# Optimization experiments

Measured on AMD Instinct MI355X. Metric: run time of the kernel, lower is better.

The kernel has to match this reference:

```python
import jax, jax.numpy as jnp
import numpy as np

LATENT = 256
OUT_CH = 1
K = 16
HEADS = 64


def _conv1x1(x, W, b):
    # x: [B, Cin, ...spatial], W: [Cout, Cin], b: [Cout]
    y = jnp.einsum('oc,bc...->bo...', W, x)
    return y + b.reshape((1, -1) + (1,) * (y.ndim - 2))


def _batch_gather(x, idx):
    # x: [B, C, N], idx: [B, Nq, K] -> [B, C, Nq, K]
    return jax.vmap(lambda xb, ib: xb[:, ib])(x, idx)


def setup_inputs() -> dict:
    key = jax.random.key(0)
    ks = jax.random.split(key, 16)
    B, N, NQ = 2, 10000, 10000
    inp = {
        'latents': jax.random.normal(ks[0], (B, LATENT, N), jnp.float32),
        'pts': jax.random.normal(ks[1], (B, 3, N), jnp.float32),
        'pts_query': jax.random.normal(ks[2], (B, 3, NQ), jnp.float32),
        'proj_ids': jax.random.randint(ks[3], (B, NQ, K), 0, N, jnp.int64),
    }
    def lin(k, o, i):
        s = 1.0 / np.sqrt(i)
        k1, k2 = jax.random.split(k)
        return (jax.random.uniform(k1, (o, i), jnp.float32, -s, s),
                jax.random.uniform(k2, (o,), jnp.float32, -s, s))
    inp['W1'], inp['b1'] = lin(ks[4], LATENT, LATENT + 3)
    inp['W2'], inp['b2'] = lin(ks[5], LATENT, LATENT)
    inp['W3'], inp['b3'] = lin(ks[6], LATENT, LATENT)
    inp['Wq'], inp['bq'] = lin(ks[7], HEADS, LATENT)
    inp['Wv'], inp['bv'] = lin(ks[8], LATENT, LATENT)
    inp['W8'], inp['b8'] = lin(ks[9], OUT_CH, LATENT)
    return inp


def reference(latents, pts, pts_query, proj_ids,
              W1, b1, W2, b2, W3, b3, Wq, bq, Wv, bv, W8, b8):
    # gather neighbor latents and points: [B, C, Nq, K], [B, 3, Nq, K]
    x = _batch_gather(latents, proj_ids)
    npts = _batch_gather(pts, proj_ids)
    rel = pts_query[:, :, :, None] - npts          # [B, 3, Nq, K]
    x = jnp.concatenate([x, rel], axis=1)          # [B, C+3, Nq, K]
    x = jax.nn.relu(_conv1x1(x, W1, b1))
    x = jax.nn.relu(_conv1x1(x, W2, b2))
    x = jax.nn.relu(_conv1x1(x, W3, b3))
    query = _conv1x1(x, Wq, bq)                    # [B, 64, Nq, K]
    value = _conv1x1(x, Wv, bv)                    # [B, C, Nq, K]
    attention = jax.nn.softmax(query, axis=-1).mean(axis=1)  # [B, Nq, K]
    # weighted sum over K neighbors: [B, Nq, C] -> [B, C, Nq]
    x = jnp.einsum('bnk,bcnk->bcn', attention, value)
    x = _conv1x1(x, W8, b8)                        # [B, out_ch, Nq]
    return x
```

## Files before the change

### kernel.cpp

```cpp
#include <hip/hip_runtime.h>
#include <cstdint>
#include <cstddef>


#define NLAT 256
#define KNB 16
#define QB 4
#define MROWS 64
#define ROWB 528
#define MTSTR 16896

typedef float    f32x4  __attribute__((ext_vector_type(4)));
typedef float    f32x16 __attribute__((ext_vector_type(16)));
typedef _Float16 f16x8  __attribute__((ext_vector_type(8)));
typedef _Float16 f16x4  __attribute__((ext_vector_type(4)));

struct Smem {
  unsigned char buf[MROWS * ROWB];
  float Sp[4][MROWS];
  float Sv[MROWS];
  int sidx[MROWS];
  int is64;
};

__device__ __forceinline__ void layer_mfma32(
    unsigned char* __restrict__ buf, const unsigned short* __restrict__ Wp,
    const float* __restrict__ bias, int lane, int wave, bool relu)
{
  const int lm32 = lane & 31, h = lane >> 5;
  const char* bp = (const char*)buf + lm32 * 528 + h * 16;
  const char* wbase = (const char*)Wp + (wave * 64 + lm32) * 32 + h * 16;

  f32x16 acc[2][2];
#pragma unroll
  for (int i = 0; i < 2; ++i)
#pragma unroll
    for (int j = 0; j < 2; ++j) acc[i][j] = (f32x16)(0.f);

#pragma unroll
  for (int ks = 0; ks < 16; ++ks) {
    f16x8 a[2], b[2];
#pragma unroll
    for (int ct = 0; ct < 2; ++ct)
      a[ct] = *(const f16x8*)(wbase + ks * 8192 + ct * 1024);
#pragma unroll
    for (int mt = 0; mt < 2; ++mt)
      b[mt] = *(const f16x8*)(bp + mt * MTSTR + ks * 32);
#pragma unroll
    for (int ct = 0; ct < 2; ++ct)
#pragma unroll
      for (int mt = 0; mt < 2; ++mt)
        acc[ct][mt] = __builtin_amdgcn_mfma_f32_32x32x16_f16(a[ct], b[mt], acc[ct][mt], 0, 0, 0);
  }
  __syncthreads();
#pragma unroll
  for (int ct = 0; ct < 2; ++ct) {
#pragma unroll
    for (int q = 0; q < 4; ++q) {
      const int ch0 = wave * 64 + ct * 32 + q * 8 + h * 4;
      const float4 bs = *(const float4*)(bias + ch0);
      const float bb[4] = {bs.x, bs.y, bs.z, bs.w};
#pragma unroll
      for (int mt = 0; mt < 2; ++mt) {
        f16x4 v;
#pragma unroll
        for (int j = 0; j < 4; ++j) {
          float x = acc[ct][mt][q * 4 + j] + bb[j];
          if (relu) x = fmaxf(x, 0.f);
          v[j] = (_Float16)x;
        }
        *(f16x4*)((char*)buf + (mt * 32 + lm32) * 528 + ch0 * 2) = v;
      }
    }
  }
}

extern "C" __global__ __launch_bounds__(256, 4)
void interp_mfma(const float* __restrict__ pts,
                 const float* __restrict__ ptsq,
                 const void*  __restrict__ proj,
                 const unsigned short* __restrict__ L1pre,
                 const float* __restrict__ w1rT,
                 const unsigned short* __restrict__ W2p,
                 const unsigned short* __restrict__ W3p,
                 const unsigned short* __restrict__ Wqh,
                 const float* __restrict__ b2, const float* __restrict__ b3,
                 const float* __restrict__ bq,
                 const float* __restrict__ wv8, const float* __restrict__ c0p,
                 float* __restrict__ out,
                 int N, int NQ)
{
  __shared__ Smem sm;
  const int tid = threadIdx.x;
  const int bid = blockIdx.x;
  const int lane = tid & 63, wave = tid >> 6;
  const int lm = lane & 15, lk = lane >> 4;

  if (tid == 0) {
    const int* p = (const int*)proj;
    int z = 1;
    for (int i = 0; i < 64; ++i) z &= (p[2 * i + 1] == 0);
    sm.is64 = z;
  }
  __syncthreads();
  if (tid < MROWS) {
    long long g = (long long)bid * QB + (tid >> 4);
    long long base = g * KNB + (tid & 15);
    sm.sidx[tid] = sm.is64 ? (int)((const long long*)proj)[base]
                           : ((const int*)proj)[base];
  }
  __syncthreads();

  {
    const int row = tid & 63, part = tid >> 6;
    const int id = sm.sidx[row];
    const long long g = (long long)bid * QB + (row >> 4);
    const int b = (int)(g / NQ);
    const int nq = (int)(g - (long long)b * NQ);
    float rel[3];
#pragma unroll
    for (int j = 0; j < 3; ++j)
      rel[j] = ptsq[((size_t)b * 3 + j) * NQ + nq]
             - pts[((size_t)b * 3 + j) * N + id];
    const _Float16* lp = (const _Float16*)L1pre + ((size_t)b * N + id) * NLAT + part * 64;
    const float* wr0 = w1rT + part * 64;
    const float* wr1 = w1rT + 256 + part * 64;
    const float* wr2 = w1rT + 512 + part * 64;
    char* dst = (char*)sm.buf + row * 528 + part * 128;
#pragma unroll
    for (int cc = 0; cc < 8; ++cc) {
      f16x8 v = *(const f16x8*)(lp + cc * 8);
      const float4 a0 = *(const float4*)(wr0 + cc * 8), a1 = *(const float4*)(wr0 + cc * 8 + 4);
      const float4 b0 = *(const float4*)(wr1 + cc * 8), b1_ = *(const float4*)(wr1 + cc * 8 + 4);
      const float4 c0 = *(const float4*)(wr2 + cc * 8), c1 = *(const float4*)(wr2 + cc * 8 + 4);
      const float wa[8] = {a0.x, a0.y, a0.z, a0.w, a1.x, a1.y, a1.z, a1.w};
      const float wb[8] = {b0.x, b0.y, b0.z, b0.w, b1_.x, b1_.y, b1_.z, b1_.w};
      const float wc[8] = {c0.x, c0.y, c0.z, c0.w, c1.x, c1.y, c1.z, c1.w};
      f16x8 o;
#pragma unroll
      for (int e = 0; e < 8; ++e) {
        float x = (float)v[e] + rel[0] * wa[e] + rel[1] * wb[e] + rel[2] * wc[e];
        o[e] = (_Float16)fmaxf(x, 0.f);
      }
      *(f16x8*)(dst + cc * 16) = o;
    }
  }
  __syncthreads();

  layer_mfma32(sm.buf, W2p, b2, lane, wave, true);
  __syncthreads();
  layer_mfma32(sm.buf, W3p, b3, lane, wave, true);
  __syncthreads();

  const char* bp16 = (const char*)sm.buf + lm * 528 + lk * 16;
  f32x4 qacc[4];
#pragma unroll
  for (int mt = 0; mt < 4; ++mt) qacc[mt] = (f32x4){0.f, 0.f, 0.f, 0.f};
  {
    const char* wqb = (const char*)Wqh + (wave * 16 + lm) * 512 + lk * 16;
#pragma unroll
    for (int ks = 0; ks < 8; ++ks) {
      f16x8 a = *(const f16x8*)(wqb + ks * 64);
#pragma unroll
      for (int mt = 0; mt < 4; ++mt) {
        f16x8 bf = *(const f16x8*)(bp16 + mt * 8448 + ks * 64);
        qacc[mt] = __builtin_amdgcn_mfma_f32_16x16x32_f16(a, bf, qacc[mt], 0, 0, 0);
      }
    }
  }
  {
    const char* sp = (const char*)sm.buf + (wave * 16 + lm) * 528 + lk * 16;
    float sacc = 0.f;
#pragma unroll
    for (int cc = 0; cc < 8; ++cc) {
      f16x8 v = *(const f16x8*)(sp + cc * 64);
      const int k0 = cc * 32 + lk * 8;
      const float4 w0 = *(const float4*)(wv8 + k0);
      const float4 w1 = *(const float4*)(wv8 + k0 + 4);
      sacc += (float)v[0] * w0.x + (float)v[1] * w0.y
            + (float)v[2] * w0.z + (float)v[3] * w0.w;
      sacc += (float)v[4] * w1.x + (float)v[5] * w1.y
            + (float)v[6] * w1.z + (float)v[7] * w1.w;
    }
    sacc += __shfl_xor(sacc, 16);
    sacc += __shfl_xor(sacc, 32);
    if (lk == 0) sm.Sv[wave * 16 + lm] = sacc;
  }

  {
    float bqv[4];
#pragma unroll
    for (int r = 0; r < 4; ++r) bqv[r] = bq[wave * 16 + lk * 4 + r];
#pragma unroll
    for (int mt = 0; mt < 4; ++mt) {
      float sw = 0.f;
#pragma unroll
      for (int r = 0; r < 4; ++r) {
        const float qv = qacc[mt][r] + bqv[r];
        float mx = qv;
#pragma unroll
        for (int msk = 1; msk < 16; msk <<= 1) mx = fmaxf(mx, __shfl_xor(mx, msk));
        const float e = __expf(qv - mx);
        float s = e;
#pragma unroll
        for (int msk = 1; msk < 16; msk <<= 1) s += __shfl_xor(s, msk);
        sw += e / s;
      }
      sw += __shfl_xor(sw, 16);
      sw += __shfl_xor(sw, 32);
      if (lk == 0) sm.Sp[wave][mt * 16 + lm] = sw;
    }
  }
  __syncthreads();

  {
    const int m = wave * 16 + lm;
    const float a = (sm.Sp[0][m] + sm.Sp[1][m] + sm.Sp[2][m] + sm.Sp[3][m]) * (1.f / 64.f);
    float val = a * sm.Sv[m];
#pragma unroll
    for (int msk = 1; msk < 16; msk <<= 1) val += __shfl_xor(val, msk);
    if (lane == 0) out[(long long)bid * QB + wave] = val + c0p[0];
  }
}

extern "C" __global__ __launch_bounds__(256, 4)
void l1pre_k(const float* __restrict__ latents,
             const unsigned short* __restrict__ W1p,
             const float* __restrict__ b1,
             unsigned short* __restrict__ L1pre, int N)
{
  __shared__ unsigned char buf[MROWS * ROWB];
  const int tid = threadIdx.x;
  const int b = blockIdx.y, n0 = blockIdx.x * 64;
  const int lane = tid & 63, wave = tid >> 6;
  const int lm32 = lane & 31, h = lane >> 5;

  {
    const int nl = tid & 63;
    const int n = n0 + nl;
    const bool ok = (n < N);
#pragma unroll
    for (int jj = 0; jj < 8; ++jj) {
      const int j = (tid >> 6) + jj * 4;
      f16x8 v;
#pragma unroll
      for (int e = 0; e < 8; ++e) {
        const float x = ok ? latents[((size_t)b * NLAT + j * 8 + e) * N + n] : 0.f;
        v[e] = (_Float16)x;
      }
      *(f16x8*)((char*)buf + nl * 528 + j * 16) = v;
    }
  }
  __syncthreads();

  const char* bp = (const char*)buf + lm32 * 528 + h * 16;
  const char* wbase = (const char*)W1p + (wave * 64 + lm32) * 32 + h * 16;
  f32x16 acc[2][2];
#pragma unroll
  for (int i = 0; i < 2; ++i)
#pragma unroll
    for (int j = 0; j < 2; ++j) acc[i][j] = (f32x16)(0.f);
#pragma unroll
  for (int ks = 0; ks < 16; ++ks) {
    f16x8 a[2], bb[2];
#pragma unroll
    for (int ct = 0; ct < 2; ++ct)
      a[ct] = *(const f16x8*)(wbase + ks * 8192 + ct * 1024);
#pragma unroll
    for (int mt = 0; mt < 2; ++mt)
      bb[mt] = *(const f16x8*)(bp + mt * MTSTR + ks * 32);
#pragma unroll
    for (int ct = 0; ct < 2; ++ct)
#pragma unroll
      for (int mt = 0; mt < 2; ++mt)
        acc[ct][mt] = __builtin_amdgcn_mfma_f32_32x32x16_f16(a[ct], bb[mt], acc[ct][mt], 0, 0, 0);
  }
#pragma unroll
  for (int ct = 0; ct < 2; ++ct) {
#pragma unroll
    for (int q = 0; q < 4; ++q) {
      const int ch0 = wave * 64 + ct * 32 + q * 8 + h * 4;
      const float4 bs = *(const float4*)(b1 + ch0);
      const float bb[4] = {bs.x, bs.y, bs.z, bs.w};
#pragma unroll
      for (int mt = 0; mt < 2; ++mt) {
        const int n = n0 + mt * 32 + lm32;
        if (n < N) {
          f16x4 v;
#pragma unroll
          for (int j = 0; j < 4; ++j)
            v[j] = (_Float16)(acc[ct][mt][q * 4 + j] + bb[j]);
          *(f16x4*)((char*)L1pre + (((size_t)b * N + n) * NLAT + ch0) * 2) = v;
        }
      }
    }
  }
}

extern "C" __global__ void prep_w(const float* __restrict__ W1, const float* __restrict__ W2,
                                  const float* __restrict__ W3, const float* __restrict__ Wq,
                                  const float* __restrict__ Wv, const float* __restrict__ W8,
                                  const float* __restrict__ bv, const float* __restrict__ b8,
                                  unsigned short* W1p, unsigned short* W2p,
                                  unsigned short* W3p, unsigned short* Wqh,
                                  float* w1rT, float* wv8, float* c0) {
  const int t = blockIdx.x * 256 + threadIdx.x;
  union { _Float16 h; unsigned short u; } cv;
  if (t < 65536) {
    const int ch = t >> 8, k = t & 255;
    const int dst = (k >> 4) * 4096 + ch * 16 + (k & 15);
    cv.h = (_Float16)W1[(size_t)ch * 259 + k]; W1p[dst] = cv.u;
    cv.h = (_Float16)W2[t]; W2p[dst] = cv.u;
    cv.h = (_Float16)W3[t]; W3p[dst] = cv.u;
  }
  if (t < 16384) { cv.h = (_Float16)Wq[t]; Wqh[t] = cv.u; }
  if (t < 768) {
    const int j = t >> 8, ch = t & 255;
    w1rT[t] = W1[(size_t)ch * 259 + 256 + j];
  }
  if (t < 256) {
    float s = 0.f;
    for (int o = 0; o < 256; ++o) s += Wv[(size_t)o * 256 + t] * W8[o];
    wv8[t] = s;
  }
  if (t < 64) {
    float s = 0.f;
#pragma unroll
    for (int i = 0; i < 4; ++i) s += bv[t + 64 * i] * W8[t + 64 * i];
#pragma unroll
    for (int msk = 1; msk < 64; msk <<= 1) s += __shfl_xor(s, msk);
    if (t == 0) c0[0] = s + b8[0];
  }
}

extern "C" void kernel_launch(void* const* d_in, const int* in_sizes, int n_in,
                              void* d_out, int out_size, void* d_ws, size_t ws_size,
                              hipStream_t stream) {
  (void)n_in; (void)out_size; (void)ws_size;
  const float* latents = (const float*)d_in[0];
  const float* pts     = (const float*)d_in[1];
  const float* ptsq    = (const float*)d_in[2];
  const void*  proj    = d_in[3];
  const float* W1 = (const float*)d_in[4];  const float* b1 = (const float*)d_in[5];
  const float* W2 = (const float*)d_in[6];  const float* b2 = (const float*)d_in[7];
  const float* W3 = (const float*)d_in[8];  const float* b3 = (const float*)d_in[9];
  const float* Wq = (const float*)d_in[10]; const float* bq = (const float*)d_in[11];
  const float* Wv = (const float*)d_in[12]; const float* bv = (const float*)d_in[13];
  const float* W8 = (const float*)d_in[14]; const float* b8 = (const float*)d_in[15];
  float* out = (float*)d_out;

  const int B  = 2;
  const int N  = in_sizes[1] / (3 * B);
  const int NQ = in_sizes[2] / (3 * B);

  size_t off = 0;
  auto alloc = [&](size_t bytes) -> char* {
    char* p = (char*)d_ws + off;
    off += (bytes + 255) & ~(size_t)255;
    return p;
  };
  unsigned short* W1p = (unsigned short*)alloc(65536 * 2);
  unsigned short* W2p = (unsigned short*)alloc(65536 * 2);
  unsigned short* W3p = (unsigned short*)alloc(65536 * 2);
  unsigned short* Wqh = (unsigned short*)alloc(16384 * 2);
  float* w1rT = (float*)alloc(768 * 4);
  float* wv8  = (float*)alloc(256 * 4);
  float* c0   = (float*)alloc(4);
  unsigned short* L1pre = (unsigned short*)alloc((size_t)B * N * NLAT * 2);

  hipLaunchKernelGGL(prep_w, dim3(256), dim3(256), 0, stream,
                     W1, W2, W3, Wq, Wv, W8, bv, b8, W1p, W2p, W3p, Wqh,
                     w1rT, wv8, c0);
  hipLaunchKernelGGL(l1pre_k, dim3((N + 63) / 64, B), dim3(256), 0, stream,
                     latents, W1p, b1, L1pre, N);
  const int nblocks = (B * NQ + QB - 1) / QB;
  hipLaunchKernelGGL(interp_mfma, dim3(nblocks), dim3(256), 0, stream,
                     pts, ptsq, proj, L1pre, w1rT, W2p, W3p, Wqh,
                     b2, b3, bq, wv8, c0, out, N, NQ);
}
```

Before: 198.2 us.

## Double block to eight waves, splitting channels and query/value work

The interp kernel now launches 512 threads per block instead of 256. In the MLP layers each wave computes 32 output channels instead of 64, and the gather covers 32 channels per thread. After layer 3, four waves do the query MFMA and softmax while the other four compute the value projection in parallel. The aim is more waves per query block, to hide gather and LDS latency. In exchange, activation tiles are re-read from LDS twice as often across waves, and the tighter launch bound squeezes registers harder.

After: 214.8 us. 1.08x slower.

```diff
diff --git a/kernel.cpp b/kernel.cpp
--- a/kernel.cpp
+++ b/kernel.cpp
@@ -29,53 +29,41 @@
 {
   const int lm32 = lane & 31, h = lane >> 5;
   const char* bp = (const char*)buf + lm32 * 528 + h * 16;
-  const char* wbase = (const char*)Wp + (wave * 64 + lm32) * 32 + h * 16;
-
-  f32x16 acc[2][2];
-#pragma unroll
-  for (int i = 0; i < 2; ++i)
-#pragma unroll
-    for (int j = 0; j < 2; ++j) acc[i][j] = (f32x16)(0.f);
+  const char* wbase = (const char*)Wp + (wave * 32 + lm32) * 32 + h * 16;
+
+  f32x16 acc[2];
+  acc[0] = (f32x16)(0.f);
+  acc[1] = (f32x16)(0.f);
 
 #pragma unroll
   for (int ks = 0; ks < 16; ++ks) {
-    f16x8 a[2], b[2];
-#pragma unroll
-    for (int ct = 0; ct < 2; ++ct)
-      a[ct] = *(const f16x8*)(wbase + ks * 8192 + ct * 1024);
-#pragma unroll
-    for (int mt = 0; mt < 2; ++mt)
-      b[mt] = *(const f16x8*)(bp + mt * MTSTR + ks * 32);
-#pragma unroll
-    for (int ct = 0; ct < 2; ++ct)
-#pragma unroll
-      for (int mt = 0; mt < 2; ++mt)
-        acc[ct][mt] = __builtin_amdgcn_mfma_f32_32x32x16_f16(a[ct], b[mt], acc[ct][mt], 0, 0, 0);
-  }
-  __syncthreads();
-#pragma unroll
-  for (int ct = 0; ct < 2; ++ct) {
-#pragma unroll
-    for (int q = 0; q < 4; ++q) {
-      const int ch0 = wave * 64 + ct * 32 + q * 8 + h * 4;
-      const float4 bs = *(const float4*)(bias + ch0);
-      const float bb[4] = {bs.x, bs.y, bs.z, bs.w};
-#pragma unroll
-      for (int mt = 0; mt < 2; ++mt) {
-        f16x4 v;
-#pragma unroll
-        for (int j = 0; j < 4; ++j) {
-          float x = acc[ct][mt][q * 4 + j] + bb[j];
-          if (relu) x = fmaxf(x, 0.f);
-          v[j] = (_Float16)x;
-        }
-        *(f16x4*)((char*)buf + (mt * 32 + lm32) * 528 + ch0 * 2) = v;
-      }
-    }
-  }
-}
-
-extern "C" __global__ __launch_bounds__(256, 4)
+    f16x8 a = *(const f16x8*)(wbase + ks * 8192);
+    f16x8 b0 = *(const f16x8*)(bp + ks * 32);
+    f16x8 b1 = *(const f16x8*)(bp + MTSTR + ks * 32);
+    acc[0] = __builtin_amdgcn_mfma_f32_32x32x16_f16(a, b0, acc[0], 0, 0, 0);
+    acc[1] = __builtin_amdgcn_mfma_f32_32x32x16_f16(a, b1, acc[1], 0, 0, 0);
+  }
+  __syncthreads();
+#pragma unroll
+  for (int q = 0; q < 4; ++q) {
+    const int ch0 = wave * 32 + q * 8 + h * 4;
+    const float4 bs = *(const float4*)(bias + ch0);
+    const float bb[4] = {bs.x, bs.y, bs.z, bs.w};
+#pragma unroll
+    for (int mt = 0; mt < 2; ++mt) {
+      f16x4 v;
+#pragma unroll
+      for (int j = 0; j < 4; ++j) {
+        float x = acc[mt][q * 4 + j] + bb[j];
+        if (relu) x = fmaxf(x, 0.f);
+        v[j] = (_Float16)x;
+      }
+      *(f16x4*)((char*)buf + (mt * 32 + lm32) * 528 + ch0 * 2) = v;
+    }
+  }
+}
+
+extern "C" __global__ __launch_bounds__(512, 8)
 void interp_mfma(const float* __restrict__ pts,
                  const float* __restrict__ ptsq,
                  const void*  __restrict__ proj,
@@ -122,13 +110,13 @@
     for (int j = 0; j < 3; ++j)
       rel[j] = ptsq[((size_t)b * 3 + j) * NQ + nq]
              - pts[((size_t)b * 3 + j) * N + id];
-    const _Float16* lp = (const _Float16*)L1pre + ((size_t)b * N + id) * NLAT + part * 64;
-    const float* wr0 = w1rT + part * 64;
-    const float* wr1 = w1rT + 256 + part * 64;
-    const float* wr2 = w1rT + 512 + part * 64;
-    char* dst = (char*)sm.buf + row * 528 + part * 128;
-#pragma unroll
-    for (int cc = 0; cc < 8; ++cc) {
+    const _Float16* lp = (const _Float16*)L1pre + ((size_t)b * N + id) * NLAT + part * 32;
+    const float* wr0 = w1rT + part * 32;
+    const float* wr1 = w1rT + 256 + part * 32;
+    const float* wr2 = w1rT + 512 + part * 32;
+    char* dst = (char*)sm.buf + row * 528 + part * 64;
+#pragma unroll
+    for (int cc = 0; cc < 4; ++cc) {
       f16x8 v = *(const f16x8*)(lp + cc * 8);
       const float4 a0 = *(const float4*)(wr0 + cc * 8), a1 = *(const float4*)(wr0 + cc * 8 + 4);
       const float4 b0 = *(const float4*)(wr1 + cc * 8), b1_ = *(const float4*)(wr1 + cc * 8 + 4);
@@ -152,24 +140,48 @@
   layer_mfma32(sm.buf, W3p, b3, lane, wave, true);
   __syncthreads();
 
-  const char* bp16 = (const char*)sm.buf + lm * 528 + lk * 16;
-  f32x4 qacc[4];
-#pragma unroll
-  for (int mt = 0; mt < 4; ++mt) qacc[mt] = (f32x4){0.f, 0.f, 0.f, 0.f};
-  {
-    const char* wqb = (const char*)Wqh + (wave * 16 + lm) * 512 + lk * 16;
-#pragma unroll
-    for (int ks = 0; ks < 8; ++ks) {
-      f16x8 a = *(const f16x8*)(wqb + ks * 64);
-#pragma unroll
-      for (int mt = 0; mt < 4; ++mt) {
-        f16x8 bf = *(const f16x8*)(bp16 + mt * 8448 + ks * 64);
-        qacc[mt] = __builtin_amdgcn_mfma_f32_16x16x32_f16(a, bf, qacc[mt], 0, 0, 0);
-      }
-    }
-  }
-  {
-    const char* sp = (const char*)sm.buf + (wave * 16 + lm) * 528 + lk * 16;
+  if (wave < 4) {
+    const char* bp16 = (const char*)sm.buf + lm * 528 + lk * 16;
+    f32x4 qacc[4];
+#pragma unroll
+    for (int mt = 0; mt < 4; ++mt) qacc[mt] = (f32x4){0.f, 0.f, 0.f, 0.f};
+    {
+      const char* wqb = (const char*)Wqh + (wave * 16 + lm) * 512 + lk * 16;
+#pragma unroll
+      for (int ks = 0; ks < 8; ++ks) {
+        f16x8 a = *(const f16x8*)(wqb + ks * 64);
+#pragma unroll
+        for (int mt = 0; mt < 4; ++mt) {
+          f16x8 bf = *(const f16x8*)(bp16 + mt * 8448 + ks * 64);
+          qacc[mt] = __builtin_amdgcn_mfma_f32_16x16x32_f16(a, bf, qacc[mt], 0, 0, 0);
+        }
+      }
+    }
+    float bqv[4];
+#pragma unroll
+    for (int r = 0; r < 4; ++r) bqv[r] = bq[wave * 16 + lk * 4 + r];
+#pragma unroll
+    for (int mt = 0; mt < 4; ++mt) {
+      float sw = 0.f;
+#pragma unroll
+      for (int r = 0; r < 4; ++r) {
+        const float qv = qacc[mt][r] + bqv[r];
+        float mx = qv;
+#pragma unroll
+        for (int msk = 1; msk < 16; msk <<= 1) mx = fmaxf(mx, __shfl_xor(mx, msk));
+        const float e = __expf(qv - mx);
+        float s = e;
+#pragma unroll
+        for (int msk = 1; msk < 16; msk <<= 1) s += __shfl_xor(s, msk);
+        sw += e / s;
+      }
+      sw += __shfl_xor(sw, 16);
+      sw += __shfl_xor(sw, 32);
+      if (lk == 0) sm.Sp[wave][mt * 16 + lm] = sw;
+    }
+  } else {
+    const int row = (wave - 4) * 16 + lm;
+    const char* sp = (const char*)sm.buf + row * 528 + lk * 16;
     float sacc = 0.f;
 #pragma unroll
     for (int cc = 0; cc < 8; ++cc) {
@@ -184,36 +196,11 @@
     }
     sacc += __shfl_xor(sacc, 16);
     sacc += __shfl_xor(sacc, 32);
-    if (lk == 0) sm.Sv[wave * 16 + lm] = sacc;
-  }
-
-  {
-    float bqv[4];
-#pragma unroll
-    for (int r = 0; r < 4; ++r) bqv[r] = bq[wave * 16 + lk * 4 + r];
-#pragma unroll
-    for (int mt = 0; mt < 4; ++mt) {
-      float sw = 0.f;
-#pragma unroll
-      for (int r = 0; r < 4; ++r) {
-        const float qv = qacc[mt][r] + bqv[r];
-        float mx = qv;
-#pragma unroll
-        for (int msk = 1; msk < 16; msk <<= 1) mx = fmaxf(mx, __shfl_xor(mx, msk));
-        const float e = __expf(qv - mx);
-        float s = e;
-#pragma unroll
-        for (int msk = 1; msk < 16; msk <<= 1) s += __shfl_xor(s, msk);
-        sw += e / s;
-      }
-      sw += __shfl_xor(sw, 16);
-      sw += __shfl_xor(sw, 32);
-      if (lk == 0) sm.Sp[wave][mt * 16 + lm] = sw;
-    }
-  }
-  __syncthreads();
-
-  {
+    if (lk == 0) sm.Sv[row] = sacc;
+  }
+  __syncthreads();
+
+  if (wave < 4) {
     const int m = wave * 16 + lm;
     const float a = (sm.Sp[0][m] + sm.Sp[1][m] + sm.Sp[2][m] + sm.Sp[3][m]) * (1.f / 64.f);
     float val = a * sm.Sv[m];
@@ -374,7 +361,7 @@
   hipLaunchKernelGGL(l1pre_k, dim3((N + 63) / 64, B), dim3(256), 0, stream,
                      latents, W1p, b1, L1pre, N);
   const int nblocks = (B * NQ + QB - 1) / QB;
-  hipLaunchKernelGGL(interp_mfma, dim3(nblocks), dim3(256), 0, stream,
+  hipLaunchKernelGGL(interp_mfma, dim3(nblocks), dim3(512), 0, stream,
                      pts, ptsq, proj, L1pre, w1rT, W2p, W3p, Wqh,
                      b2, b3, bq, wv8, c0, out, N, NQ);
 }
```
